# Performance work log

Hardware: AMD Instinct MI355X
Metric: run time of the kernel (lower is better)

Reference implementation:

```python
import jax, jax.numpy as jnp
import numpy as np

# Model dims: batch, num_patches, patch_dim, emb_dim, heads, layers, ffn, vocab, grid
B, N, PD, D, H, L, F, V, G = 4, 1024, 768, 768, 12, 6, 3072, 1024, 32
HD = D // H  # head dim = 64


def setup_inputs() -> dict:
    key = jax.random.key(0)
    ks = jax.random.split(key, 22)
    s = 0.02
    r = lambda k, shp: jax.random.normal(k, shp, dtype=jnp.float32) * s
    return {
        "patches": jax.random.normal(ks[0], (B, N, PD), dtype=jnp.float32),
        "mask": jax.random.bernoulli(ks[1], 0.3, (B, N)),
        "mask_token": r(ks[2], (PD,)),
        "patch_w": r(ks[3], (D, PD)),
        "patch_b": jnp.zeros((D,), jnp.float32),
        "pos_emb": r(ks[4], (N, D)),
        "rel_bias": r(ks[5], (2 * G - 1, 2 * G - 1)),
        # stacked per-layer params [L, ...]
        "in_w": r(ks[6], (L, 3 * D, D)),
        "in_b": jnp.zeros((L, 3 * D), jnp.float32),
        "attn_ow": r(ks[7], (L, D, D)),
        "attn_ob": jnp.zeros((L, D), jnp.float32),
        "ln1_s": jnp.ones((L, D), jnp.float32),
        "ln1_b": jnp.zeros((L, D), jnp.float32),
        "ffn_w1": r(ks[8], (L, F, D)),
        "ffn_b1": jnp.zeros((L, F), jnp.float32),
        "ffn_w2": r(ks[9], (L, D, F)),
        "ffn_b2": jnp.zeros((L, D), jnp.float32),
        "ln2_s": jnp.ones((L, D), jnp.float32),
        "ln2_b": jnp.zeros((L, D), jnp.float32),
        "head_w": r(ks[10], (V, D)),
        "head_b": jnp.zeros((V,), jnp.float32),
    }


def _layer_norm(x, scale, bias, eps=1e-5):
    mu = jnp.mean(x, axis=-1, keepdims=True)
    var = jnp.mean(jnp.square(x - mu), axis=-1, keepdims=True)
    return (x - mu) * jax.lax.rsqrt(var + eps) * scale + bias


def _rel_bias(rel_bias):
    # gathered Swin-style relative position bias -> [N, N]
    idx = jnp.arange(N)
    rows, cols = idx // G, idx % G
    ir = rows[:, None] - rows[None, :] + (G - 1)
    ic = cols[:, None] - cols[None, :] + (G - 1)
    return rel_bias[ir, ic]


def reference(patches, mask, mask_token, patch_w, patch_b, pos_emb, rel_bias,
              in_w, in_b, attn_ow, attn_ob, ln1_s, ln1_b,
              ffn_w1, ffn_b1, ffn_w2, ffn_b2, ln2_s, ln2_b, head_w, head_b):
    # replace masked patches with mask_token, project, add abs pos emb
    x = jnp.where(mask[:, :, None], mask_token, patches)
    x = x @ patch_w.T + patch_b + pos_emb  # [B,N,D]
    bias = _rel_bias(rel_bias)  # [N,N] additive attention bias
    scale = 1.0 / np.sqrt(HD).astype(np.float32)
    for l in range(L):
        qkv = x @ in_w[l].T + in_b[l]  # [B,N,3D]
        q, k, v = jnp.split(qkv, 3, axis=-1)
        split_heads = lambda t: t.reshape(B, N, H, HD).transpose(0, 2, 1, 3)
        q, k, v = split_heads(q), split_heads(k), split_heads(v)
        scores = jnp.einsum('bhqd,bhkd->bhqk', q, k) * scale + bias
        attn = jax.nn.softmax(scores, axis=-1)
        o = jnp.einsum('bhqk,bhkd->bhqd', attn, v)
        o = o.transpose(0, 2, 1, 3).reshape(B, N, D) @ attn_ow[l].T + attn_ob[l]
        x = _layer_norm(x + o, ln1_s[l], ln1_b[l])
        h = jax.nn.gelu(x @ ffn_w1[l].T + ffn_b1[l], approximate=False)
        x = _layer_norm(x + h @ ffn_w2[l].T + ffn_b2[l], ln2_s[l], ln2_b[l])
    logits = x @ head_w.T + head_b  # [B,N,V] (dropout = identity in eval)
    return logits, mask
```

## Files before the change

kernel.cpp:

```cpp
#include <hip/hip_runtime.h>
#include <hip/hip_bf16.h>
#include <stdint.h>


#define BM 64
#define BN 64
#define BK 32

using u16 = unsigned short;
typedef __attribute__((ext_vector_type(8))) short short8;
typedef __attribute__((ext_vector_type(4))) float f32x4;
typedef __attribute__((ext_vector_type(4))) u16 u16x4;

#define GPTR(p) ((const __attribute__((address_space(1))) void*)(p))
#define LPTR(p) ((__attribute__((address_space(3))) void*)(p))

__device__ __forceinline__ float b2f(u16 u){
  union { unsigned int i; float f; } x; x.i = ((unsigned int)u) << 16; return x.f;
}
__device__ __forceinline__ u16 f2b(float f){
  f = fminf(fmaxf(f, -448.0f), 448.0f);
  union { float f; unsigned int i; } x; x.f = f;
  unsigned int r = x.i + 0x7FFFu + ((x.i >> 16) & 1u);
  return (u16)(r >> 16);
}

__global__ __launch_bounds__(256) void detect_k(const u16* __restrict__ mk, int* __restrict__ mode){
  __shared__ int f[3];
  int tid = threadIdx.x;
  if (tid < 3) f[tid] = 0;
  __syncthreads();
  for (int i = tid; i < 2048; i += 256){
    u16 u = mk[i];
    if (u == 256 || u == 257) atomicOr(&f[0], 1);
    if (u == 0x3F80){ if ((i & 1) == 0) atomicOr(&f[1], 1); else atomicOr(&f[2], 1); }
  }
  __syncthreads();
  if (tid == 0){
    int m;
    if (f[0]) m = 0;
    else if (f[1]) m = 1;
    else if (f[2]) m = 2;
    else m = 3;
    *mode = m;
  }
}

__device__ __forceinline__ bool mask_at(const void* mk, int mode, int i){
  if (mode == 0) return ((const unsigned char*)mk)[i] != 0;
  if (mode == 1) return ((const u16*)mk)[i] != 0;
  if (mode == 2) return ((const float*)mk)[i] != 0.0f;
  return ((const int*)mk)[i] != 0;
}

__global__ __launch_bounds__(256) void wconv_k(const float* __restrict__ src, u16* __restrict__ dst){
  long i = ((long)blockIdx.x * 256 + threadIdx.x) * 4;
  float4 v = *(const float4*)(src + i);
  u16x4 o; o.x = f2b(v.x); o.y = f2b(v.y); o.z = f2b(v.z); o.w = f2b(v.w);
  *(u16x4*)(dst + i) = o;
}

__global__ __launch_bounds__(256) void embed_k(const float* __restrict__ patches, const void* __restrict__ mask,
                                               const int* __restrict__ mode, const float* __restrict__ mtok,
                                               u16* __restrict__ MP){
  int row = blockIdx.x;
  bool m = mask_at(mask, *mode, row);
  int tid = threadIdx.x;
  long base = (long)row * 768;
  #pragma unroll
  for (int i = 0; i < 3; i++){
    int p = tid + i * 256;
    MP[base + p] = f2b(m ? mtok[p] : patches[base + p]);
  }
}

__global__ __launch_bounds__(256) void maskout_k(const void* __restrict__ mask, const int* __restrict__ mode,
                                                 float* __restrict__ out){
  int i = blockIdx.x * 256 + threadIdx.x;
  out[i] = mask_at(mask, *mode, i) ? 1.0f : 0.0f;
}

__global__ __launch_bounds__(256) void ln_k(const u16* __restrict__ XR, u16* __restrict__ X,
                                            const float* __restrict__ s, const float* __restrict__ b){
  int row = blockIdx.x;
  int tid = threadIdx.x;
  const u16* xr = XR + (long)row * 768;
  float v0 = b2f(xr[tid]), v1 = b2f(xr[tid + 256]), v2 = b2f(xr[tid + 512]);
  float sum = v0 + v1 + v2, sq = v0 * v0 + v1 * v1 + v2 * v2;
  #pragma unroll
  for (int off = 32; off; off >>= 1){ sum += __shfl_xor(sum, off); sq += __shfl_xor(sq, off); }
  __shared__ float ls[4], lq[4];
  int wave = tid >> 6, lane = tid & 63;
  if (lane == 0){ ls[wave] = sum; lq[wave] = sq; }
  __syncthreads();
  sum = ls[0] + ls[1] + ls[2] + ls[3];
  sq  = lq[0] + lq[1] + lq[2] + lq[3];
  float mu = sum * (1.0f / 768.0f);
  float var = fmaxf(sq * (1.0f / 768.0f) - mu * mu, 0.0f);
  float rs = rsqrtf(var + 1e-5f);
  u16* xo = X + (long)row * 768;
  xo[tid]       = f2b((v0 - mu) * rs * s[tid]       + b[tid]);
  xo[tid + 256] = f2b((v1 - mu) * rs * s[tid + 256] + b[tid + 256]);
  xo[tid + 512] = f2b((v2 - mu) * rs * s[tid + 512] + b[tid + 512]);
}

struct GP {
  const u16* A; const u16* W; u16* C; float* Cf;
  const float* bias; const float* pose;
  const u16* resid;
  u16* Cv;
  long sAz, sWz;
  int lda, ldw, ldc;
  int N, K;
  int wclamp, zBase;
};

template<int EPI>
__global__ __launch_bounds__(256)
void gemm_k(GP g){
  __shared__ __align__(16) u16 As[3][BM * BK];
  __shared__ __align__(16) u16 Bs[3][BN * BK];
  const int tid  = threadIdx.x;
  const int wave = tid >> 6, lane = tid & 63;
  const int quad = lane >> 4, l16 = lane & 15;
  const int wm = wave >> 1, wn = wave & 1;

  const int gx = gridDim.x;
  const int nwg = gx * gridDim.y;
  int bid = blockIdx.y * gx + blockIdx.x;
  {
    const int q = nwg >> 3, r = nwg & 7;
    const int xcd = bid & 7, loc = bid >> 3;
    bid = (xcd < r ? xcd * (q + 1) : r * (q + 1) + (xcd - r) * q) + loc;
  }
  const int m0 = (bid / gx) * BM;
  const int n0 = (bid % gx) * BN;
  const int z = blockIdx.z;

  const u16* Ab = g.A + (long)z * g.sAz;
  const u16* Wb = g.W + (long)z * g.sWz;

  f32x4 acc[2][2];
  #pragma unroll
  for (int i = 0; i < 2; i++)
    #pragma unroll
    for (int j = 0; j < 2; j++) acc[i][j] = (f32x4){0.f, 0.f, 0.f, 0.f};

  const int c0 = wave * 64 + lane;
  const int arow = c0 >> 2, aslot = (c0 & 3) ^ ((arow >> 1) & 3);
  const u16* a0 = Ab + (long)(m0 + arow) * g.lda + aslot * 8;
  const u16* w0 = Wb + (long)min(n0 + arow, g.wclamp) * g.ldw + aslot * 8;
  const int o0 = wave * 512;

  const int nt = g.K / BK;
  const int rs = (quad ^ ((l16 >> 1) & 3)) * 8;

  #define STAGE(sb, kt) do { \
    __builtin_amdgcn_global_load_lds(GPTR(a0 + (kt)), LPTR(&As[(sb)][o0]), 16, 0, 0); \
    __builtin_amdgcn_global_load_lds(GPTR(w0 + (kt)), LPTR(&Bs[(sb)][o0]), 16, 0, 0); \
  } while (0)

  STAGE(0, 0);
  if (nt > 1){
    STAGE(1, BK);
    asm volatile("s_waitcnt vmcnt(2)\n\ts_barrier" ::: "memory");
  } else {
    asm volatile("s_waitcnt vmcnt(0)\n\ts_barrier" ::: "memory");
  }

  int sC = 0, sP = 2;
  for (int t = 0; t < nt; ++t){
    if (t + 2 < nt) STAGE(sP, (t + 2) * BK);

    short8 af[2], bf[2];
    af[0] = *(const short8*)&As[sC][(wm * 32 + l16) * BK + rs];
    af[1] = *(const short8*)&As[sC][(wm * 32 + 16 + l16) * BK + rs];
    bf[0] = *(const short8*)&Bs[sC][(wn * 32 + l16) * BK + rs];
    bf[1] = *(const short8*)&Bs[sC][(wn * 32 + 16 + l16) * BK + rs];
    acc[0][0] = __builtin_amdgcn_mfma_f32_16x16x32_bf16(af[0], bf[0], acc[0][0], 0, 0, 0);
    acc[0][1] = __builtin_amdgcn_mfma_f32_16x16x32_bf16(af[0], bf[1], acc[0][1], 0, 0, 0);
    acc[1][0] = __builtin_amdgcn_mfma_f32_16x16x32_bf16(af[1], bf[0], acc[1][0], 0, 0, 0);
    acc[1][1] = __builtin_amdgcn_mfma_f32_16x16x32_bf16(af[1], bf[1], acc[1][1], 0, 0, 0);

    if (t + 2 < nt)      asm volatile("s_waitcnt vmcnt(2) lgkmcnt(0)\n\ts_barrier" ::: "memory");
    else if (t + 1 < nt) asm volatile("s_waitcnt vmcnt(0) lgkmcnt(0)\n\ts_barrier" ::: "memory");
    sC = (sC == 2) ? 0 : sC + 1;
    sP = (sP == 2) ? 0 : sP + 1;
  }
  #undef STAGE

  #pragma unroll
  for (int i = 0; i < 2; i++){
    #pragma unroll
    for (int j = 0; j < 2; j++){
      #pragma unroll
      for (int rr = 0; rr < 4; rr++){
        const long r = (long)m0 + wm * 32 + i * 16 + quad * 4 + rr;
        const int  c = n0 + wn * 32 + j * 16 + l16;
        if (c >= g.N) continue;
        float v = acc[i][j][rr];
        if constexpr (EPI == 0){
          u16 o = f2b(v + g.bias[c]);
          if (c < 1536) g.C[r * 1536 + c] = o;
          else {
            int c2 = c - 1536;
            int hh = ((int)(r >> 10)) * 12 + (c2 >> 6);
            g.Cv[((long)hh * 64 + (c2 & 63)) * 1024 + (r & 1023)] = o;
          }
        } else if constexpr (EPI == 3){
          long o = r * (long)g.ldc + c;
          g.C[o] = f2b(v + g.bias[c] + b2f(g.resid[o]));
        } else if constexpr (EPI == 4){
          float t2 = v + g.bias[c];
          g.C[r * (long)g.ldc + c] = f2b(0.5f * t2 * (1.0f + erff(t2 * 0.70710678118654752f)));
        } else if constexpr (EPI == 5){
          float t2 = v + g.bias[c];
          t2 = fminf(fmaxf(t2, -1.0e4f), 1.0e4f);
          g.Cf[r * (long)g.ldc + c] = t2;
        } else {
          float val = v + g.bias[c] + g.pose[(long)(r & 1023) * 768 + c];
          g.C[r * (long)g.ldc + c] = f2b(val);
        }
      }
    }
  }
}

static inline void glaunch(int epi, dim3 grid, const GP& g, hipStream_t stream){
  switch (epi){
    case 0: gemm_k<0><<<grid, dim3(256), 0, stream>>>(g); break;
    case 3: gemm_k<3><<<grid, dim3(256), 0, stream>>>(g); break;
    case 4: gemm_k<4><<<grid, dim3(256), 0, stream>>>(g); break;
    case 5: gemm_k<5><<<grid, dim3(256), 0, stream>>>(g); break;
    default: gemm_k<6><<<grid, dim3(256), 0, stream>>>(g); break;
  }
}

struct FP {
  const u16* QK; const u16* VT; u16* O; const float* relb;
  int oBase;
};

__global__ __launch_bounds__(256) void flash_k(FP f){
  __shared__ __align__(16) u16 Qs[2][2048];
  __shared__ __align__(16) u16 Ks[2][2][2048];
  __shared__ __align__(16) u16 Vs[2][2][2048];
  __shared__ __align__(16) u16 Ps[2][2048];
  __shared__ float rmx[64][2], rsm[64][2];
  const int tid  = threadIdx.x;
  const int wave = tid >> 6, lane = tid & 63;
  const int quad = lane >> 4, l16 = lane & 15;
  const int wm = wave >> 1, wn = wave & 1;
  const int hhl = blockIdx.y, bl = hhl / 12, h = hhl - bl * 12;
  const int q0 = blockIdx.x * 64;

  const int srow = tid >> 2, sslot = (tid & 3) ^ ((srow >> 1) & 3);
  const u16* Qsrc = f.QK + ((long)bl * 1024 + q0 + srow) * 1536 + h * 64 + sslot * 8;
  const u16* Ksrc = f.QK + ((long)bl * 1024 + srow) * 1536 + 768 + h * 64 + sslot * 8;
  const u16* Vsrc = f.VT + ((long)hhl * 64 + srow) * 1024 + sslot * 8;
  const int od = wave * 512;
  const int rs = (quad ^ ((l16 >> 1) & 3)) * 8;

  __builtin_amdgcn_global_load_lds(GPTR(Qsrc),      LPTR(&Qs[0][od]),    16, 0, 0);
  __builtin_amdgcn_global_load_lds(GPTR(Qsrc + 32), LPTR(&Qs[1][od]),    16, 0, 0);
  __builtin_amdgcn_global_load_lds(GPTR(Ksrc),      LPTR(&Ks[0][0][od]), 16, 0, 0);
  __builtin_amdgcn_global_load_lds(GPTR(Ksrc + 32), LPTR(&Ks[0][1][od]), 16, 0, 0);
  __builtin_amdgcn_global_load_lds(GPTR(Vsrc),      LPTR(&Vs[0][0][od]), 16, 0, 0);
  __builtin_amdgcn_global_load_lds(GPTR(Vsrc + 32), LPTR(&Vs[0][1][od]), 16, 0, 0);
  asm volatile("s_waitcnt vmcnt(0) lgkmcnt(0)\n\ts_barrier" ::: "memory");

  f32x4 Oa[2][2];
  #pragma unroll
  for (int i = 0; i < 2; i++)
    #pragma unroll
    for (int j = 0; j < 2; j++) Oa[i][j] = (f32x4){0.f, 0.f, 0.f, 0.f};
  float m_[2][4], l_[2][4];
  #pragma unroll
  for (int i = 0; i < 2; i++)
    #pragma unroll
    for (int rr = 0; rr < 4; rr++){ m_[i][rr] = -1e30f; l_[i][rr] = 0.0f; }

  for (int t = 0; t < 16; ++t){
    const int cur = t & 1;
    if (t < 15){
      const u16* kn = Ksrc + (long)(t + 1) * 98304;
      const u16* vn = Vsrc + (t + 1) * 64;
      __builtin_amdgcn_global_load_lds(GPTR(kn),      LPTR(&Ks[cur ^ 1][0][od]), 16, 0, 0);
      __builtin_amdgcn_global_load_lds(GPTR(kn + 32), LPTR(&Ks[cur ^ 1][1][od]), 16, 0, 0);
      __builtin_amdgcn_global_load_lds(GPTR(vn),      LPTR(&Vs[cur ^ 1][0][od]), 16, 0, 0);
      __builtin_amdgcn_global_load_lds(GPTR(vn + 32), LPTR(&Vs[cur ^ 1][1][od]), 16, 0, 0);
    }

    f32x4 S[2][2];
    #pragma unroll
    for (int i = 0; i < 2; i++)
      #pragma unroll
      for (int j = 0; j < 2; j++) S[i][j] = (f32x4){0.f, 0.f, 0.f, 0.f};
    #pragma unroll
    for (int ks = 0; ks < 2; ks++){
      short8 af[2], bf[2];
      af[0] = *(const short8*)&Qs[ks][(wm * 32 + l16) * 32 + rs];
      af[1] = *(const short8*)&Qs[ks][(wm * 32 + 16 + l16) * 32 + rs];
      bf[0] = *(const short8*)&Ks[cur][ks][(wn * 32 + l16) * 32 + rs];
      bf[1] = *(const short8*)&Ks[cur][ks][(wn * 32 + 16 + l16) * 32 + rs];
      S[0][0] = __builtin_amdgcn_mfma_f32_16x16x32_bf16(af[0], bf[0], S[0][0], 0, 0, 0);
      S[0][1] = __builtin_amdgcn_mfma_f32_16x16x32_bf16(af[0], bf[1], S[0][1], 0, 0, 0);
      S[1][0] = __builtin_amdgcn_mfma_f32_16x16x32_bf16(af[1], bf[0], S[1][0], 0, 0, 0);
      S[1][1] = __builtin_amdgcn_mfma_f32_16x16x32_bf16(af[1], bf[1], S[1][1], 0, 0, 0);
    }

    float tmax[2][4];
    #pragma unroll
    for (int i = 0; i < 2; i++)
      #pragma unroll
      for (int rr = 0; rr < 4; rr++) tmax[i][rr] = -1e30f;
    #pragma unroll
    for (int i = 0; i < 2; i++){
      #pragma unroll
      for (int j = 0; j < 2; j++){
        #pragma unroll
        for (int rr = 0; rr < 4; rr++){
          const int qy = wm * 32 + i * 16 + quad * 4 + rr;
          const int kx = t * 64 + wn * 32 + j * 16 + l16;
          const int ir = ((q0 + qy) >> 5) - (kx >> 5) + 31;
          const int ic = (qy & 31) - (kx & 31) + 31;
          float s = S[i][j][rr] * 0.125f + f.relb[ir * 63 + ic];
          S[i][j][rr] = s;
          tmax[i][rr] = fmaxf(tmax[i][rr], s);
        }
      }
    }
    #pragma unroll
    for (int i = 0; i < 2; i++)
      #pragma unroll
      for (int rr = 0; rr < 4; rr++)
        #pragma unroll
        for (int off = 1; off < 16; off <<= 1)
          tmax[i][rr] = fmaxf(tmax[i][rr], __shfl_xor(tmax[i][rr], off));
    if (l16 == 0){
      #pragma unroll
      for (int i = 0; i < 2; i++)
        #pragma unroll
        for (int rr = 0; rr < 4; rr++)
          rmx[wm * 32 + i * 16 + quad * 4 + rr][wn] = tmax[i][rr];
    }
    asm volatile("s_waitcnt lgkmcnt(0)\n\ts_barrier" ::: "memory");

    float psum[2][4];
    #pragma unroll
    for (int i = 0; i < 2; i++){
      #pragma unroll
      for (int rr = 0; rr < 4; rr++){
        const int row = wm * 32 + i * 16 + quad * 4 + rr;
        const float tm = fmaxf(rmx[row][0], rmx[row][1]);
        const float mn = fmaxf(m_[i][rr], tm);
        const float sc = __expf(m_[i][rr] - mn);
        m_[i][rr] = mn; l_[i][rr] *= sc;
        #pragma unroll
        for (int j = 0; j < 2; j++) Oa[i][j][rr] *= sc;
        psum[i][rr] = 0.0f;
      }
    }
    #pragma unroll
    for (int i = 0; i < 2; i++){
      #pragma unroll
      for (int j = 0; j < 2; j++){
        #pragma unroll
        for (int rr = 0; rr < 4; rr++){
          float p = __expf(S[i][j][rr] - m_[i][rr]);
          psum[i][rr] += p;
          const int row = wm * 32 + i * 16 + quad * 4 + rr;
          const int col = wn * 32 + j * 16 + l16;
          const int half = col >> 5, c5 = col & 31;
          const int ps = (c5 >> 3) ^ ((row >> 1) & 3);
          Ps[half][row * 32 + ps * 8 + (c5 & 7)] = f2b(p);
        }
      }
    }
    #pragma unroll
    for (int i = 0; i < 2; i++)
      #pragma unroll
      for (int rr = 0; rr < 4; rr++)
        #pragma unroll
        for (int off = 1; off < 16; off <<= 1)
          psum[i][rr] += __shfl_xor(psum[i][rr], off);
    if (l16 == 0){
      #pragma unroll
      for (int i = 0; i < 2; i++)
        #pragma unroll
        for (int rr = 0; rr < 4; rr++)
          rsm[wm * 32 + i * 16 + quad * 4 + rr][wn] = psum[i][rr];
    }
    asm volatile("s_waitcnt lgkmcnt(0)\n\ts_barrier" ::: "memory");
    #pragma unroll
    for (int i = 0; i < 2; i++)
      #pragma unroll
      for (int rr = 0; rr < 4; rr++){
        const int row = wm * 32 + i * 16 + quad * 4 + rr;
        l_[i][rr] += rsm[row][0] + rsm[row][1];
      }

    #pragma unroll
    for (int ks = 0; ks < 2; ks++){
      short8 pa[2], bv[2];
      pa[0] = *(const short8*)&Ps[ks][(wm * 32 + l16) * 32 + rs];
      pa[1] = *(const short8*)&Ps[ks][(wm * 32 + 16 + l16) * 32 + rs];
      bv[0] = *(const short8*)&Vs[cur][ks][(wn * 32 + l16) * 32 + rs];
      bv[1] = *(const short8*)&Vs[cur][ks][(wn * 32 + 16 + l16) * 32 + rs];
      Oa[0][0] = __builtin_amdgcn_mfma_f32_16x16x32_bf16(pa[0], bv[0], Oa[0][0], 0, 0, 0);
      Oa[0][1] = __builtin_amdgcn_mfma_f32_16x16x32_bf16(pa[0], bv[1], Oa[0][1], 0, 0, 0);
      Oa[1][0] = __builtin_amdgcn_mfma_f32_16x16x32_bf16(pa[1], bv[0], Oa[1][0], 0, 0, 0);
      Oa[1][1] = __builtin_amdgcn_mfma_f32_16x16x32_bf16(pa[1], bv[1], Oa[1][1], 0, 0, 0);
    }
    if (t < 15) asm volatile("s_waitcnt vmcnt(0) lgkmcnt(0)\n\ts_barrier" ::: "memory");
  }

  #pragma unroll
  for (int i = 0; i < 2; i++){
    #pragma unroll
    for (int rr = 0; rr < 4; rr++){
      const float inv = 1.0f / l_[i][rr];
      const int row = wm * 32 + i * 16 + quad * 4 + rr;
      const long ro = ((long)(f.oBase + bl) * 1024 + q0 + row) * 768 + h * 64;
      #pragma unroll
      for (int j = 0; j < 2; j++)
        f.O[ro + wn * 32 + j * 16 + l16] = f2b(Oa[i][j][rr] * inv);
    }
  }
}

extern "C" void kernel_launch(void* const* d_in, const int* in_sizes, int n_in,
                              void* d_out, int out_size, void* d_ws, size_t ws_size,
                              hipStream_t stream){
  (void)in_sizes; (void)n_in; (void)out_size;
  const float* patches = (const float*)d_in[0];
  const void*  mask    = d_in[1];
  const float* mtok    = (const float*)d_in[2];
  const float* patch_w = (const float*)d_in[3];
  const float* patch_b = (const float*)d_in[4];
  const float* pos_emb = (const float*)d_in[5];
  const float* rel_b   = (const float*)d_in[6];
  const float* in_w    = (const float*)d_in[7];
  const float* in_b    = (const float*)d_in[8];
  const float* attn_ow = (const float*)d_in[9];
  const float* attn_ob = (const float*)d_in[10];
  const float* ln1_s   = (const float*)d_in[11];
  const float* ln1_b   = (const float*)d_in[12];
  const float* ffn_w1  = (const float*)d_in[13];
  const float* ffn_b1  = (const float*)d_in[14];
  const float* ffn_w2  = (const float*)d_in[15];
  const float* ffn_b2  = (const float*)d_in[16];
  const float* ln2_s   = (const float*)d_in[17];
  const float* ln2_b   = (const float*)d_in[18];
  const float* head_w  = (const float*)d_in[19];
  const float* head_b  = (const float*)d_in[20];

  char* ws = (char*)d_ws;
  int* mode = (int*)ws;
  u16* X  = (u16*)(ws + 256);
  u16* WA = X + 3145728;
  u16* WB = WA + 2359296;
  char* EX = (char*)(WB + 2359296);
  long extra = (long)ws_size - 15728896L;
  const bool bigWs = extra >= 25165824L;

  u16*   dout16 = (u16*)d_out;
  float* doutf  = (float*)d_out;

  u16* QKp = (u16*)EX;
  u16* VTp = QKp + 6291456;
  u16* Op  = VTp + 3145728;
  u16* Hp  = (u16*)EX;
  u16* O16  = dout16;
  u16* QKh  = dout16 + 3145728;
  u16* VTh  = dout16 + 6291456;
  u16* XRb  = dout16 + 3145728;
  u16* Hc   = dout16;
  u16* XRc  = dout16 + 6291456;

  detect_k<<<dim3(1), dim3(256), 0, stream>>>((const u16*)mask, mode);

  GP g; FP fp;
  wconv_k<<<dim3(576), dim3(256), 0, stream>>>(patch_w, WA);
  embed_k<<<dim3(4096), dim3(256), 0, stream>>>(patches, mask, mode, mtok, dout16);
  g = {};
  g.A = dout16; g.lda = 768; g.W = WA; g.ldw = 768; g.wclamp = 767;
  g.C = X; g.ldc = 768; g.N = 768; g.K = 768;
  g.bias = patch_b; g.pose = pos_emb;
  glaunch(6, dim3(12, 64, 1), g, stream);

  for (int l = 0; l < 6; l++){
    wconv_k<<<dim3(1728), dim3(256), 0, stream>>>(in_w + (long)l * 1769472, WA);
    wconv_k<<<dim3(576),  dim3(256), 0, stream>>>(attn_ow + (long)l * 589824, WB);

    if (bigWs){
      g = {};
      g.A = X; g.lda = 768; g.W = WA; g.ldw = 768; g.wclamp = 2303;
      g.bias = in_b + (long)l * 2304;
      g.C = QKp; g.Cv = VTp; g.N = 2304; g.K = 768;
      glaunch(0, dim3(36, 64, 1), g, stream);

      fp = {};
      fp.QK = QKp; fp.VT = VTp; fp.O = Op; fp.relb = rel_b; fp.oBase = 0;
      flash_k<<<dim3(16, 48), dim3(256), 0, stream>>>(fp);

      g = {};
      g.A = Op; g.lda = 768; g.W = WB; g.ldw = 768; g.wclamp = 767;
      g.bias = attn_ob + (long)l * 768; g.resid = X;
      g.C = dout16; g.ldc = 768; g.N = 768; g.K = 768;
      glaunch(3, dim3(12, 64, 1), g, stream);
      ln_k<<<dim3(4096), dim3(256), 0, stream>>>(dout16, X, ln1_s + l * 768, ln1_b + l * 768);
    } else {
      for (int hb = 0; hb < 2; hb++){
        g = {};
        g.A = X + (long)hb * 1572864; g.lda = 768;
        g.W = WA; g.ldw = 768; g.wclamp = 2303;
        g.bias = in_b + (long)l * 2304;
        g.C = QKh; g.Cv = VTh; g.N = 2304; g.K = 768;
        glaunch(0, dim3(36, 32, 1), g, stream);

        fp = {};
        fp.QK = QKh; fp.VT = VTh; fp.O = O16; fp.relb = rel_b; fp.oBase = hb * 2;
        flash_k<<<dim3(16, 24), dim3(256), 0, stream>>>(fp);
      }
      g = {};
      g.A = O16; g.lda = 768; g.W = WB; g.ldw = 768; g.wclamp = 767;
      g.bias = attn_ob + (long)l * 768; g.resid = X;
      g.C = XRb; g.ldc = 768; g.N = 768; g.K = 768;
      glaunch(3, dim3(12, 64, 1), g, stream);
      ln_k<<<dim3(4096), dim3(256), 0, stream>>>(XRb, X, ln1_s + l * 768, ln1_b + l * 768);
    }

    wconv_k<<<dim3(2304), dim3(256), 0, stream>>>(ffn_w1 + (long)l * 2359296, WA);
    wconv_k<<<dim3(2304), dim3(256), 0, stream>>>(ffn_w2 + (long)l * 2359296, WB);

    if (bigWs){
      g = {};
      g.A = X; g.lda = 768; g.W = WA; g.ldw = 768; g.wclamp = 3071;
      g.bias = ffn_b1 + (long)l * 3072;
      g.C = Hp; g.ldc = 3072; g.N = 3072; g.K = 768;
      glaunch(4, dim3(48, 64, 1), g, stream);
      g = {};
      g.A = Hp; g.lda = 3072; g.W = WB; g.ldw = 3072; g.wclamp = 767;
      g.bias = ffn_b2 + (long)l * 768; g.resid = X;
      g.C = dout16; g.ldc = 768; g.N = 768; g.K = 3072;
      glaunch(3, dim3(12, 64, 1), g, stream);
      ln_k<<<dim3(4096), dim3(256), 0, stream>>>(dout16, X, ln2_s + l * 768, ln2_b + l * 768);
    } else {
      for (int cc = 0; cc < 2; cc++){
        u16* Xc = X + (long)cc * 1572864;
        g = {};
        g.A = Xc; g.lda = 768; g.W = WA; g.ldw = 768; g.wclamp = 3071;
        g.bias = ffn_b1 + (long)l * 3072;
        g.C = Hc; g.ldc = 3072; g.N = 3072; g.K = 768;
        glaunch(4, dim3(48, 32, 1), g, stream);
        g = {};
        g.A = Hc; g.lda = 3072; g.W = WB; g.ldw = 3072; g.wclamp = 767;
        g.bias = ffn_b2 + (long)l * 768; g.resid = Xc;
        g.C = XRc; g.ldc = 768; g.N = 768; g.K = 3072;
        glaunch(3, dim3(12, 32, 1), g, stream);
        ln_k<<<dim3(2048), dim3(256), 0, stream>>>(XRc, Xc, ln2_s + l * 768, ln2_b + l * 768);
      }
    }
  }

  wconv_k<<<dim3(768), dim3(256), 0, stream>>>(head_w, WA);
  g = {};
  g.A = X; g.lda = 768; g.W = WA; g.ldw = 768; g.wclamp = 1023;
  g.bias = head_b;
  g.Cf = doutf; g.ldc = 1024; g.N = 1024; g.K = 768;
  glaunch(5, dim3(16, 64, 1), g, stream);
  maskout_k<<<dim3(16), dim3(256), 0, stream>>>(mask, mode, doutf + 4194304);
}
```

Baseline: 1.855 ms.

## Transpose flash attention tiles so softmax reductions become per-lane, add XCD-aware remap

Computes S^T = K·Q^T and O^T = V·P^T so that each lane owns one query column. The softmax max and sum then reduce with two cross-quad shuffles instead of four-step 16-lane butterflies over eight rows. The relative-bias loads become one 4-wide vector load per fragment, P is packed to bf16 with v_cvt_pk_bf16_f32, and output stores are 4-wide. It also remaps workgroup ids so consecutive q-tiles of the same head land on the same XCD, aiming for better L2 reuse of K/V. The trade-offs are more intricate indexing, a possible difference in bf16 rounding and clamping of P, and unaligned float4 loads of the bias.

New measurement: 1.647 ms. -11.3%, faster.

```diff
diff --git a/kernel.cpp b/kernel.cpp
--- a/kernel.cpp
+++ b/kernel.cpp
@@ -11,6 +11,7 @@
 typedef __attribute__((ext_vector_type(8))) short short8;
 typedef __attribute__((ext_vector_type(4))) float f32x4;
 typedef __attribute__((ext_vector_type(4))) u16 u16x4;
+typedef float f32x4u __attribute__((ext_vector_type(4), aligned(4)));
 
 #define GPTR(p) ((const __attribute__((address_space(1))) void*)(p))
 #define LPTR(p) ((__attribute__((address_space(3))) void*)(p))
@@ -23,6 +24,11 @@
   union { float f; unsigned int i; } x; x.f = f;
   unsigned int r = x.i + 0x7FFFu + ((x.i >> 16) & 1u);
   return (u16)(r >> 16);
+}
+__device__ __forceinline__ unsigned int cvtpk(float lo, float hi){
+  unsigned int r;
+  asm("v_cvt_pk_bf16_f32 %0, %1, %2" : "=v"(r) : "v"(lo), "v"(hi));
+  return r;
 }
 
 __global__ __launch_bounds__(256) void detect_k(const u16* __restrict__ mk, int* __restrict__ mode){
@@ -251,8 +257,17 @@
   const int wave = tid >> 6, lane = tid & 63;
   const int quad = lane >> 4, l16 = lane & 15;
   const int wm = wave >> 1, wn = wave & 1;
-  const int hhl = blockIdx.y, bl = hhl / 12, h = hhl - bl * 12;
-  const int q0 = blockIdx.x * 64;
+
+  {
+  }
+  const int nwg = gridDim.x * gridDim.y;
+  int orig = blockIdx.y * gridDim.x + blockIdx.x;
+  const int q_ = nwg >> 3, r_ = nwg & 7;
+  const int xcd = orig & 7, loc = orig >> 3;
+  const int nid = (xcd < r_ ? xcd * (q_ + 1) : r_ * (q_ + 1) + (xcd - r_) * q_) + loc;
+  const int hhl = nid >> 4;
+  const int q0  = (nid & 15) * 64;
+  const int bl = hhl / 12, h = hhl - bl * 12;
 
   const int srow = tid >> 2, sslot = (tid & 3) ^ ((srow >> 1) & 3);
   const u16* Qsrc = f.QK + ((long)bl * 1024 + q0 + srow) * 1536 + h * 64 + sslot * 8;
@@ -274,11 +289,17 @@
   for (int i = 0; i < 2; i++)
     #pragma unroll
     for (int j = 0; j < 2; j++) Oa[i][j] = (f32x4){0.f, 0.f, 0.f, 0.f};
-  float m_[2][4], l_[2][4];
+  float m_[2] = {-1e30f, -1e30f}, l_[2] = {0.0f, 0.0f};
+
+  const int qloc0 = wn * 32 + l16, qloc1 = qloc0 + 16;
+  const int qr = (q0 >> 5) + wn;
+  const float* brbase = f.relb + (long)(qr - wm + 31) * 63;
+  int ic3[2][2];
   #pragma unroll
   for (int i = 0; i < 2; i++)
     #pragma unroll
-    for (int rr = 0; rr < 4; rr++){ m_[i][rr] = -1e30f; l_[i][rr] = 0.0f; }
+    for (int j = 0; j < 2; j++)
+      ic3[i][j] = (j * 16 + l16) - (i * 16 + quad * 4) + 28;
 
   for (int t = 0; t < 16; ++t){
     const int cur = t & 1;
@@ -291,140 +312,118 @@
       __builtin_amdgcn_global_load_lds(GPTR(vn + 32), LPTR(&Vs[cur ^ 1][1][od]), 16, 0, 0);
     }
 
-    f32x4 S[2][2];
+    f32x4 ST[2][2];
     #pragma unroll
     for (int i = 0; i < 2; i++)
       #pragma unroll
-      for (int j = 0; j < 2; j++) S[i][j] = (f32x4){0.f, 0.f, 0.f, 0.f};
-    #pragma unroll
-    for (int ks = 0; ks < 2; ks++){
-      short8 af[2], bf[2];
-      af[0] = *(const short8*)&Qs[ks][(wm * 32 + l16) * 32 + rs];
-      af[1] = *(const short8*)&Qs[ks][(wm * 32 + 16 + l16) * 32 + rs];
-      bf[0] = *(const short8*)&Ks[cur][ks][(wn * 32 + l16) * 32 + rs];
-      bf[1] = *(const short8*)&Ks[cur][ks][(wn * 32 + 16 + l16) * 32 + rs];
-      S[0][0] = __builtin_amdgcn_mfma_f32_16x16x32_bf16(af[0], bf[0], S[0][0], 0, 0, 0);
-      S[0][1] = __builtin_amdgcn_mfma_f32_16x16x32_bf16(af[0], bf[1], S[0][1], 0, 0, 0);
-      S[1][0] = __builtin_amdgcn_mfma_f32_16x16x32_bf16(af[1], bf[0], S[1][0], 0, 0, 0);
-      S[1][1] = __builtin_amdgcn_mfma_f32_16x16x32_bf16(af[1], bf[1], S[1][1], 0, 0, 0);
-    }
-
-    float tmax[2][4];
-    #pragma unroll
-    for (int i = 0; i < 2; i++)
-      #pragma unroll
-      for (int rr = 0; rr < 4; rr++) tmax[i][rr] = -1e30f;
+      for (int j = 0; j < 2; j++) ST[i][j] = (f32x4){0.f, 0.f, 0.f, 0.f};
+    #pragma unroll
+    for (int ds = 0; ds < 2; ds++){
+      short8 kf[2], qf[2];
+      kf[0] = *(const short8*)&Ks[cur][ds][(wm * 32 + l16) * 32 + rs];
+      kf[1] = *(const short8*)&Ks[cur][ds][(wm * 32 + 16 + l16) * 32 + rs];
+      qf[0] = *(const short8*)&Qs[ds][(wn * 32 + l16) * 32 + rs];
+      qf[1] = *(const short8*)&Qs[ds][(wn * 32 + 16 + l16) * 32 + rs];
+      ST[0][0] = __builtin_amdgcn_mfma_f32_16x16x32_bf16(kf[0], qf[0], ST[0][0], 0, 0, 0);
+      ST[0][1] = __builtin_amdgcn_mfma_f32_16x16x32_bf16(kf[0], qf[1], ST[0][1], 0, 0, 0);
+      ST[1][0] = __builtin_amdgcn_mfma_f32_16x16x32_bf16(kf[1], qf[0], ST[1][0], 0, 0, 0);
+      ST[1][1] = __builtin_amdgcn_mfma_f32_16x16x32_bf16(kf[1], qf[1], ST[1][1], 0, 0, 0);
+    }
+
+    const float* br = brbase - (long)(2 * t) * 63;
+    float s[2][2][4];
+    float tmax0 = -1e30f, tmax1 = -1e30f;
     #pragma unroll
     for (int i = 0; i < 2; i++){
       #pragma unroll
       for (int j = 0; j < 2; j++){
+        f32x4u bv = *(const f32x4u*)(br + ic3[i][j]);
         #pragma unroll
         for (int rr = 0; rr < 4; rr++){
-          const int qy = wm * 32 + i * 16 + quad * 4 + rr;
-          const int kx = t * 64 + wn * 32 + j * 16 + l16;
-          const int ir = ((q0 + qy) >> 5) - (kx >> 5) + 31;
-          const int ic = (qy & 31) - (kx & 31) + 31;
-          float s = S[i][j][rr] * 0.125f + f.relb[ir * 63 + ic];
-          S[i][j][rr] = s;
-          tmax[i][rr] = fmaxf(tmax[i][rr], s);
+          float sv = ST[i][j][rr] * 0.125f + bv[3 - rr];
+          s[i][j][rr] = sv;
+          if (j == 0) tmax0 = fmaxf(tmax0, sv); else tmax1 = fmaxf(tmax1, sv);
         }
       }
     }
-    #pragma unroll
-    for (int i = 0; i < 2; i++)
-      #pragma unroll
-      for (int rr = 0; rr < 4; rr++)
-        #pragma unroll
-        for (int off = 1; off < 16; off <<= 1)
-          tmax[i][rr] = fmaxf(tmax[i][rr], __shfl_xor(tmax[i][rr], off));
-    if (l16 == 0){
-      #pragma unroll
-      for (int i = 0; i < 2; i++)
-        #pragma unroll
-        for (int rr = 0; rr < 4; rr++)
-          rmx[wm * 32 + i * 16 + quad * 4 + rr][wn] = tmax[i][rr];
-    }
+    tmax0 = fmaxf(tmax0, __shfl_xor(tmax0, 16));
+    tmax0 = fmaxf(tmax0, __shfl_xor(tmax0, 32));
+    tmax1 = fmaxf(tmax1, __shfl_xor(tmax1, 16));
+    tmax1 = fmaxf(tmax1, __shfl_xor(tmax1, 32));
+    if (quad == 0){ rmx[qloc0][wm] = tmax0; rmx[qloc1][wm] = tmax1; }
     asm volatile("s_waitcnt lgkmcnt(0)\n\ts_barrier" ::: "memory");
 
-    float psum[2][4];
+    float sc0, sc1;
+    {
+      float mn = fmaxf(m_[0], fmaxf(rmx[qloc0][0], rmx[qloc0][1]));
+      sc0 = __expf(m_[0] - mn); m_[0] = mn;
+    }
+    {
+      float mn = fmaxf(m_[1], fmaxf(rmx[qloc1][0], rmx[qloc1][1]));
+      sc1 = __expf(m_[1] - mn); m_[1] = mn;
+    }
+    l_[0] *= sc0; l_[1] *= sc1;
     #pragma unroll
     for (int i = 0; i < 2; i++){
       #pragma unroll
-      for (int rr = 0; rr < 4; rr++){
-        const int row = wm * 32 + i * 16 + quad * 4 + rr;
-        const float tm = fmaxf(rmx[row][0], rmx[row][1]);
-        const float mn = fmaxf(m_[i][rr], tm);
-        const float sc = __expf(m_[i][rr] - mn);
-        m_[i][rr] = mn; l_[i][rr] *= sc;
-        #pragma unroll
-        for (int j = 0; j < 2; j++) Oa[i][j][rr] *= sc;
-        psum[i][rr] = 0.0f;
-      }
-    }
+      for (int rr = 0; rr < 4; rr++){ Oa[i][0][rr] *= sc0; Oa[i][1][rr] *= sc1; }
+    }
+
+    float ps0 = 0.0f, ps1 = 0.0f;
     #pragma unroll
     for (int i = 0; i < 2; i++){
       #pragma unroll
       for (int j = 0; j < 2; j++){
-        #pragma unroll
-        for (int rr = 0; rr < 4; rr++){
-          float p = __expf(S[i][j][rr] - m_[i][rr]);
-          psum[i][rr] += p;
-          const int row = wm * 32 + i * 16 + quad * 4 + rr;
-          const int col = wn * 32 + j * 16 + l16;
-          const int half = col >> 5, c5 = col & 31;
-          const int ps = (c5 >> 3) ^ ((row >> 1) & 3);
-          Ps[half][row * 32 + ps * 8 + (c5 & 7)] = f2b(p);
-        }
+        const float mj = j ? m_[1] : m_[0];
+        float p0 = __expf(s[i][j][0] - mj);
+        float p1 = __expf(s[i][j][1] - mj);
+        float p2 = __expf(s[i][j][2] - mj);
+        float p3 = __expf(s[i][j][3] - mj);
+        float s4 = (p0 + p1) + (p2 + p3);
+        if (j == 0) ps0 += s4; else ps1 += s4;
+        const int qq = j ? qloc1 : qloc0;
+        const int sw = (i * 2 + (quad >> 1)) ^ ((qq >> 1) & 3);
+        uint2 w; w.x = cvtpk(p0, p1); w.y = cvtpk(p2, p3);
+        *(uint2*)&Ps[wm][qq * 32 + sw * 8 + (quad & 1) * 4] = w;
       }
     }
-    #pragma unroll
-    for (int i = 0; i < 2; i++)
-      #pragma unroll
-      for (int rr = 0; rr < 4; rr++)
-        #pragma unroll
-        for (int off = 1; off < 16; off <<= 1)
-          psum[i][rr] += __shfl_xor(psum[i][rr], off);
-    if (l16 == 0){
-      #pragma unroll
-      for (int i = 0; i < 2; i++)
-        #pragma unroll
-        for (int rr = 0; rr < 4; rr++)
-          rsm[wm * 32 + i * 16 + quad * 4 + rr][wn] = psum[i][rr];
-    }
+    ps0 += __shfl_xor(ps0, 16); ps0 += __shfl_xor(ps0, 32);
+    ps1 += __shfl_xor(ps1, 16); ps1 += __shfl_xor(ps1, 32);
+    if (quad == 0){ rsm[qloc0][wm] = ps0; rsm[qloc1][wm] = ps1; }
     asm volatile("s_waitcnt lgkmcnt(0)\n\ts_barrier" ::: "memory");
-    #pragma unroll
-    for (int i = 0; i < 2; i++)
-      #pragma unroll
-      for (int rr = 0; rr < 4; rr++){
-        const int row = wm * 32 + i * 16 + quad * 4 + rr;
-        l_[i][rr] += rsm[row][0] + rsm[row][1];
-      }
+    l_[0] += rsm[qloc0][0] + rsm[qloc0][1];
+    l_[1] += rsm[qloc1][0] + rsm[qloc1][1];
 
     #pragma unroll
     for (int ks = 0; ks < 2; ks++){
-      short8 pa[2], bv[2];
-      pa[0] = *(const short8*)&Ps[ks][(wm * 32 + l16) * 32 + rs];
-      pa[1] = *(const short8*)&Ps[ks][(wm * 32 + 16 + l16) * 32 + rs];
-      bv[0] = *(const short8*)&Vs[cur][ks][(wn * 32 + l16) * 32 + rs];
-      bv[1] = *(const short8*)&Vs[cur][ks][(wn * 32 + 16 + l16) * 32 + rs];
-      Oa[0][0] = __builtin_amdgcn_mfma_f32_16x16x32_bf16(pa[0], bv[0], Oa[0][0], 0, 0, 0);
-      Oa[0][1] = __builtin_amdgcn_mfma_f32_16x16x32_bf16(pa[0], bv[1], Oa[0][1], 0, 0, 0);
-      Oa[1][0] = __builtin_amdgcn_mfma_f32_16x16x32_bf16(pa[1], bv[0], Oa[1][0], 0, 0, 0);
-      Oa[1][1] = __builtin_amdgcn_mfma_f32_16x16x32_bf16(pa[1], bv[1], Oa[1][1], 0, 0, 0);
+      short8 vf[2], pf[2];
+      vf[0] = *(const short8*)&Vs[cur][ks][(wm * 32 + l16) * 32 + rs];
+      vf[1] = *(const short8*)&Vs[cur][ks][(wm * 32 + 16 + l16) * 32 + rs];
+      pf[0] = *(const short8*)&Ps[ks][(wn * 32 + l16) * 32 + rs];
+      pf[1] = *(const short8*)&Ps[ks][(wn * 32 + 16 + l16) * 32 + rs];
+      Oa[0][0] = __builtin_amdgcn_mfma_f32_16x16x32_bf16(vf[0], pf[0], Oa[0][0], 0, 0, 0);
+      Oa[0][1] = __builtin_amdgcn_mfma_f32_16x16x32_bf16(vf[0], pf[1], Oa[0][1], 0, 0, 0);
+      Oa[1][0] = __builtin_amdgcn_mfma_f32_16x16x32_bf16(vf[1], pf[0], Oa[1][0], 0, 0, 0);
+      Oa[1][1] = __builtin_amdgcn_mfma_f32_16x16x32_bf16(vf[1], pf[1], Oa[1][1], 0, 0, 0);
     }
     if (t < 15) asm volatile("s_waitcnt vmcnt(0) lgkmcnt(0)\n\ts_barrier" ::: "memory");
   }
 
+  const float inv0 = 1.0f / l_[0], inv1 = 1.0f / l_[1];
   #pragma unroll
   for (int i = 0; i < 2; i++){
     #pragma unroll
-    for (int rr = 0; rr < 4; rr++){
-      const float inv = 1.0f / l_[i][rr];
-      const int row = wm * 32 + i * 16 + quad * 4 + rr;
-      const long ro = ((long)(f.oBase + bl) * 1024 + q0 + row) * 768 + h * 64;
-      #pragma unroll
-      for (int j = 0; j < 2; j++)
-        f.O[ro + wn * 32 + j * 16 + l16] = f2b(Oa[i][j][rr] * inv);
+    for (int j = 0; j < 2; j++){
+      const float invj = j ? inv1 : inv0;
+      const int qq = j ? qloc1 : qloc0;
+      const long ro = ((long)(f.oBase + bl) * 1024 + q0 + qq) * 768 + h * 64
+                    + wm * 32 + i * 16 + quad * 4;
+      u16x4 o;
+      o.x = f2b(Oa[i][j][0] * invj);
+      o.y = f2b(Oa[i][j][1] * invj);
+      o.z = f2b(Oa[i][j][2] * invj);
+      o.w = f2b(Oa[i][j][3] * invj);
+      *(u16x4*)&f.O[ro] = o;
     }
   }
 }
```
